# Performance work log

Measured on AMD Instinct MI355X. Metric: run time of the kernel, lower is better.

## Reference

```python
import jax, jax.numpy as jnp
import numpy as np

EPS = 1e-5


def setup_inputs() -> dict:
    key = jax.random.key(0)
    k1, k2, k3, k4 = jax.random.split(key, 4)
    B, C, H, W = 4, 64, 128, 256
    Hg, Wg = 512, 1024
    NC = 19  # num_class; loop also covers ignore label 255 -> NC+1 entries
    x = jax.random.normal(k1, (B, C, H, W), dtype=jnp.float32)
    gt = jax.random.randint(k2, (B, Hg, Wg), 0, 19).astype(jnp.int32)
    eps_mu = jax.random.normal(k3, (NC + 1, B, C), dtype=jnp.float32)
    eps_std = jax.random.normal(k4, (NC + 1, B, C), dtype=jnp.float32)
    return {"x": x, "gt": gt, "eps_mu": eps_mu, "eps_std": eps_std}


def _sqrtvar(t):
    # torch .var(dim=0) is unbiased (ddof=1); repeat over batch is just broadcast
    return jnp.sqrt(jnp.var(t, axis=0, ddof=1, keepdims=True) + EPS)


def reference(x, gt, eps_mu, eps_std):
    B, C, H, W = x.shape
    NC1 = eps_mu.shape[0]  # num_class + 1 (ignore label 255)
    Hg, Wg = gt.shape[1], gt.shape[2]
    # nearest resize of the (binary) mask == compare on nearest-resized labels
    # torch F.interpolate nearest: src = floor(dst * in/out)
    ih = (jnp.arange(H) * Hg) // H
    iw = (jnp.arange(W) * Wg) // W
    gt_r = gt[:, ih[:, None], iw[None, :]]  # [B,H,W]
    class_ids = jnp.concatenate(
        [jnp.arange(NC1 - 1), jnp.array([255])]).astype(gt.dtype)

    def per_class(carry, inp):
        cid, emu, estd = inp
        mask = (gt_r == cid).astype(x.dtype)[:, None]  # [B,1,H,W]
        mx = x * mask
        npx = jnp.sum(mask, axis=(2, 3))               # [B,1]
        npx = jnp.where(npx == 0, jnp.ones_like(npx), npx)
        mean = jnp.sum(mx, axis=(2, 3)) / npx          # [B,C] == mean*wh/npx
        var = jnp.sum((mask * (mx - mean[:, :, None, None])) ** 2,
                      axis=(2, 3)) / npx
        std = jnp.sqrt(var + EPS)                      # [B,C]
        beta = mean + emu * _sqrtvar(mean)
        gamma = std + estd * _sqrtvar(std)
        xn = (mx - mean[:, :, None, None]) / std[:, :, None, None]
        out = mask * (xn * gamma[:, :, None, None] + beta[:, :, None, None])
        return carry + out, None

    class_x, _ = jax.lax.scan(per_class, jnp.zeros_like(x),
                              (class_ids, eps_mu, eps_std))
    return class_x
```

## Files before the change

kernel.cpp:

```cpp
#include <hip/hip_runtime.h>

#define EPS 1e-5f
constexpr int B = 4, C = 64, H = 128, W = 256;
constexpr int Hg = 512, Wg = 1024;
constexpr int NC = 19;
constexpr int HW = H * W;
constexpr int HW4 = HW / 4;

__global__ __launch_bounds__(256) void k_pack(const int* __restrict__ gt,
                                              unsigned int* __restrict__ gt_p,
                                              int* __restrict__ counts_pb) {
  __shared__ int hist[NC];
  int t = threadIdx.x;
  if (t < NC) hist[t] = 0;
  __syncthreads();
  int R = blockIdx.x * 4 + (t >> 6);
  int ws = t & 63;
  int b = R >> 7, h = R & 127;
  const int* row = gt + (size_t)(b * Hg + h * 4) * Wg;
  unsigned int c0 = (unsigned int)row[ws * 16 + 0];
  unsigned int c1 = (unsigned int)row[ws * 16 + 4];
  unsigned int c2 = (unsigned int)row[ws * 16 + 8];
  unsigned int c3 = (unsigned int)row[ws * 16 + 12];
  gt_p[R * 64 + ws] = c0 | (c1 << 8) | (c2 << 16) | (c3 << 24);
  atomicAdd(&hist[c0], 1); atomicAdd(&hist[c1], 1);
  atomicAdd(&hist[c2], 1); atomicAdd(&hist[c3], 1);
  __syncthreads();
  if (t < NC) counts_pb[t * 128 + blockIdx.x] = hist[t];
}

__global__ __launch_bounds__(256, 4) void k_stats(const float* __restrict__ x,
                                                  const unsigned int* __restrict__ gt_p,
                                                  const int* __restrict__ counts_pb,
                                                  float2* __restrict__ par,
                                                  int* __restrict__ counts) {
  int t = threadIdx.x;
  int plane = blockIdx.x >> 2;
  int q = blockIdx.x & 3;
  int b = plane >> 6, c = plane & 63;

  if (c == 0 && q == 0 && t < NC) {
    const int4* cp = (const int4*)&counts_pb[t * 128 + b * 32];
    int s = 0;
#pragma unroll
    for (int j = 0; j < 8; j++) { int4 cv = cp[j]; s += cv.x + cv.y + cv.z + cv.w; }
    counts[b * NC + t] = s;
  }

  float accS[NC], accQ[NC];
#pragma unroll
  for (int k = 0; k < NC; k++) { accS[k] = 0.f; accQ[k] = 0.f; }

  const float4* xp = (const float4*)x + (size_t)plane * (HW / 4) + q * 2048;
  const unsigned int* gp = gt_p + (size_t)b * HW4 + q * 2048;
  for (int j = 0; j < 8; j++) {
    int i = j * 256 + t;
    float4 v = xp[i];
    unsigned int g = gp[i];
    int c0 = g & 255, c1 = (g >> 8) & 255, c2 = (g >> 16) & 255, c3 = g >> 24;
#pragma unroll
    for (int k = 0; k < NC; k++) {
      float m0 = (c0 == k) ? v.x : 0.f;
      float m1 = (c1 == k) ? v.y : 0.f;
      float m2 = (c2 == k) ? v.z : 0.f;
      float m3 = (c3 == k) ? v.w : 0.f;
      accS[k] += (m0 + m1) + (m2 + m3);
      accQ[k] += fmaf(m0, m0, fmaf(m1, m1, fmaf(m2, m2, m3 * m3)));
    }
  }

#pragma unroll
  for (int k = 0; k < NC; k++) {
    float s = accS[k], qq = accQ[k];
    for (int m = 32; m >= 1; m >>= 1) {
      s  += __shfl_xor(s, m, 64);
      qq += __shfl_xor(qq, m, 64);
    }
    accS[k] = s; accQ[k] = qq;
  }
  if ((t & 63) == 0) {
    int w = t >> 6;
#pragma unroll
    for (int k = 0; k < NC; k++) {
      int e = (k * B + b) * C + c;
      par[e * 16 + q * 4 + w] = make_float2(accS[k], accQ[k]);
    }
  }
}

__global__ __launch_bounds__(256) void k_apply(const float* __restrict__ x,
                                               const unsigned int* __restrict__ gt_p,
                                               const float2* __restrict__ par,
                                               const int* __restrict__ counts,
                                               const float* __restrict__ eps_mu,
                                               const float* __restrict__ eps_std,
                                               float* __restrict__ out) {
  __shared__ float2 tab[NC];
  int t = threadIdx.x;
  int plane = blockIdx.x >> 2;
  int q = blockIdx.x & 3;
  int b = plane >> 6, c = plane & 63;
  const float4* xp = (const float4*)x + (size_t)plane * (HW / 4) + q * 2048;
  const unsigned int* gp = gt_p + (size_t)b * HW4 + q * 2048;
  float4* op = (float4*)out + (size_t)plane * (HW / 4) + q * 2048;

  float4 v0 = xp[t];
  unsigned int g0 = gp[t];

  if (t < NC) {
    float mean[B], stdv[B];
    float msum = 0.f, ssum = 0.f;
#pragma unroll
    for (int bb = 0; bb < B; bb++) {
      int cnt = counts[bb * NC + t];
      float n = cnt > 0 ? (float)cnt : 1.f;
      const float4* pp = (const float4*)&par[((t * B + bb) * C + c) * 16];
      float s = 0.f, qq = 0.f;
#pragma unroll
      for (int j = 0; j < 8; j++) { float4 p = pp[j]; s += p.x + p.z; qq += p.y + p.w; }
      float m = s / n;
      float var = qq / n - m * m;
      var = var > 0.f ? var : 0.f;
      mean[bb] = m;
      stdv[bb] = sqrtf(var + EPS);
      msum += m; ssum += stdv[bb];
    }
    float mbar = msum * 0.25f, sbar = ssum * 0.25f;
    float vm = 0.f, vs = 0.f;
#pragma unroll
    for (int bb = 0; bb < B; bb++) {
      float dm = mean[bb] - mbar; vm += dm * dm;
      float ds = stdv[bb] - sbar; vs += ds * ds;
    }
    float sqvm = sqrtf(vm * (1.f / 3.f) + EPS);
    float sqvs = sqrtf(vs * (1.f / 3.f) + EPS);
    int e = (t * B + b) * C + c;
    float beta  = mean[b] + eps_mu[e]  * sqvm;
    float gamma = stdv[b] + eps_std[e] * sqvs;
    float sc = gamma / stdv[b];
    tab[t] = make_float2(sc, beta - mean[b] * sc);
  }
  __syncthreads();

  {
    float2 a0 = tab[g0 & 255], a1 = tab[(g0 >> 8) & 255];
    float2 a2 = tab[(g0 >> 16) & 255], a3 = tab[g0 >> 24];
    float4 o;
    o.x = fmaf(v0.x, a0.x, a0.y);
    o.y = fmaf(v0.y, a1.x, a1.y);
    o.z = fmaf(v0.z, a2.x, a2.y);
    o.w = fmaf(v0.w, a3.x, a3.y);
    op[t] = o;
  }
  for (int j = 1; j < 8; j++) {
    int i = j * 256 + t;
    float4 v = xp[i];
    unsigned int g = gp[i];
    float2 a0 = tab[g & 255], a1 = tab[(g >> 8) & 255];
    float2 a2 = tab[(g >> 16) & 255], a3 = tab[g >> 24];
    float4 o;
    o.x = fmaf(v.x, a0.x, a0.y);
    o.y = fmaf(v.y, a1.x, a1.y);
    o.z = fmaf(v.z, a2.x, a2.y);
    o.w = fmaf(v.w, a3.x, a3.y);
    op[i] = o;
  }
}

extern "C" void kernel_launch(void* const* d_in, const int* in_sizes, int n_in,
                              void* d_out, int out_size, void* d_ws, size_t ws_size,
                              hipStream_t stream) {
  const float* x       = (const float*)d_in[0];
  const int*   gt      = (const int*)  d_in[1];
  const float* eps_mu  = (const float*)d_in[2];
  const float* eps_std = (const float*)d_in[3];
  float* out = (float*)d_out;

  char* ws = (char*)d_ws;
  unsigned int* gt_p     = (unsigned int*)(ws);
  int*          counts_pb= (int*)   (ws + 131072);
  int*          counts   = (int*)   (ws + 140800);
  float2*       par      = (float2*)(ws + 141104);

  hipLaunchKernelGGL(k_pack,  dim3(B * H / 4), dim3(256), 0, stream, gt, gt_p, counts_pb);
  hipLaunchKernelGGL(k_stats, dim3(B * C * 4), dim3(256), 0, stream,
                     x, gt_p, counts_pb, par, counts);
  hipLaunchKernelGGL(k_apply, dim3(B * C * 4), dim3(256), 0, stream,
                     x, gt_p, par, counts, eps_mu, eps_std, out);
}
```

Before: 119.8 us.

## Fuse pack, stats and apply into one cooperative kernel with grid syncs

Merges the three kernels into a single cooperative launch of 512 blocks. Two grid-wide barriers replace the kernel boundaries, and each block now handles half a plane instead of a quarter. The goal is to cut launch gaps between kernels and to keep each block's slice of x warm in cache between the stats pass and the apply pass. In exchange it adds cooperative-launch constraints and grid.sync cost, and there are fewer blocks to hide latency.

```diff
diff --git a/kernel.cpp b/kernel.cpp
--- a/kernel.cpp
+++ b/kernel.cpp
@@ -1,4 +1,7 @@
 #include <hip/hip_runtime.h>
+#include <hip/hip_cooperative_groups.h>
+
+namespace cg = cooperative_groups;
 
 #define EPS 1e-5f
 constexpr int B = 4, C = 64, H = 128, W = 256;
@@ -7,39 +10,44 @@
 constexpr int HW = H * W;
 constexpr int HW4 = HW / 4;
 
-__global__ __launch_bounds__(256) void k_pack(const int* __restrict__ gt,
-                                              unsigned int* __restrict__ gt_p,
-                                              int* __restrict__ counts_pb) {
+__global__ __launch_bounds__(256, 2) void k_fused(const float* __restrict__ x,
+                                                  const int* __restrict__ gt,
+                                                  const float* __restrict__ eps_mu,
+                                                  const float* __restrict__ eps_std,
+                                                  float* __restrict__ out,
+                                                  unsigned int* __restrict__ gt_p,
+                                                  int* __restrict__ counts_pb,
+                                                  int* __restrict__ counts,
+                                                  float2* __restrict__ par) {
+  cg::grid_group grid = cg::this_grid();
   __shared__ int hist[NC];
+  __shared__ float2 tab[NC];
   int t = threadIdx.x;
-  if (t < NC) hist[t] = 0;
-  __syncthreads();
-  int R = blockIdx.x * 4 + (t >> 6);
-  int ws = t & 63;
-  int b = R >> 7, h = R & 127;
-  const int* row = gt + (size_t)(b * Hg + h * 4) * Wg;
-  unsigned int c0 = (unsigned int)row[ws * 16 + 0];
-  unsigned int c1 = (unsigned int)row[ws * 16 + 4];
-  unsigned int c2 = (unsigned int)row[ws * 16 + 8];
-  unsigned int c3 = (unsigned int)row[ws * 16 + 12];
-  gt_p[R * 64 + ws] = c0 | (c1 << 8) | (c2 << 16) | (c3 << 24);
-  atomicAdd(&hist[c0], 1); atomicAdd(&hist[c1], 1);
-  atomicAdd(&hist[c2], 1); atomicAdd(&hist[c3], 1);
-  __syncthreads();
-  if (t < NC) counts_pb[t * 128 + blockIdx.x] = hist[t];
-}
+  int blk = blockIdx.x;
+  int plane = blk >> 1;
+  int half = blk & 1;
+  int b = plane >> 6, c = plane & 63;
+  int lane = t & 63, w = t >> 6;
 
-__global__ __launch_bounds__(256, 4) void k_stats(const float* __restrict__ x,
-                                                  const unsigned int* __restrict__ gt_p,
-                                                  const int* __restrict__ counts_pb,
-                                                  float2* __restrict__ par,
-                                                  int* __restrict__ counts) {
-  int t = threadIdx.x;
-  int plane = blockIdx.x >> 2;
-  int q = blockIdx.x & 3;
-  int b = plane >> 6, c = plane & 63;
+  if (blk < 128) {
+    if (t < NC) hist[t] = 0;
+    __syncthreads();
+    int R = blk * 4 + w;
+    int bb = R >> 7, h = R & 127;
+    const int* row = gt + (size_t)(bb * Hg + h * 4) * Wg;
+    unsigned int c0 = (unsigned int)row[lane * 16 + 0];
+    unsigned int c1 = (unsigned int)row[lane * 16 + 4];
+    unsigned int c2 = (unsigned int)row[lane * 16 + 8];
+    unsigned int c3 = (unsigned int)row[lane * 16 + 12];
+    gt_p[R * 64 + lane] = c0 | (c1 << 8) | (c2 << 16) | (c3 << 24);
+    atomicAdd(&hist[c0], 1); atomicAdd(&hist[c1], 1);
+    atomicAdd(&hist[c2], 1); atomicAdd(&hist[c3], 1);
+    __syncthreads();
+    if (t < NC) counts_pb[t * 128 + blk] = hist[t];
+  }
+  grid.sync();
 
-  if (c == 0 && q == 0 && t < NC) {
+  if (c == 0 && half == 0 && t < NC) {
     const int4* cp = (const int4*)&counts_pb[t * 128 + b * 32];
     int s = 0;
 #pragma unroll
@@ -51,9 +59,9 @@
 #pragma unroll
   for (int k = 0; k < NC; k++) { accS[k] = 0.f; accQ[k] = 0.f; }
 
-  const float4* xp = (const float4*)x + (size_t)plane * (HW / 4) + q * 2048;
-  const unsigned int* gp = gt_p + (size_t)b * HW4 + q * 2048;
-  for (int j = 0; j < 8; j++) {
+  const float4* xp = (const float4*)x + (size_t)plane * (HW / 4) + half * 4096;
+  const unsigned int* gp = gt_p + (size_t)b * HW4 + half * 4096;
+  for (int j = 0; j < 16; j++) {
     int i = j * 256 + t;
     float4 v = xp[i];
     unsigned int g = gp[i];
@@ -68,7 +76,6 @@
       accQ[k] += fmaf(m0, m0, fmaf(m1, m1, fmaf(m2, m2, m3 * m3)));
     }
   }
-
 #pragma unroll
   for (int k = 0; k < NC; k++) {
     float s = accS[k], qq = accQ[k];
@@ -78,32 +85,16 @@
     }
     accS[k] = s; accQ[k] = qq;
   }
-  if ((t & 63) == 0) {
-    int w = t >> 6;
+  if (lane == 0) {
 #pragma unroll
     for (int k = 0; k < NC; k++) {
       int e = (k * B + b) * C + c;
-      par[e * 16 + q * 4 + w] = make_float2(accS[k], accQ[k]);
+      par[e * 8 + half * 4 + w] = make_float2(accS[k], accQ[k]);
     }
   }
-}
+  grid.sync();
 
-__global__ __launch_bounds__(256) void k_apply(const float* __restrict__ x,
-                                               const unsigned int* __restrict__ gt_p,
-                                               const float2* __restrict__ par,
-                                               const int* __restrict__ counts,
-                                               const float* __restrict__ eps_mu,
-                                               const float* __restrict__ eps_std,
-                                               float* __restrict__ out) {
-  __shared__ float2 tab[NC];
-  int t = threadIdx.x;
-  int plane = blockIdx.x >> 2;
-  int q = blockIdx.x & 3;
-  int b = plane >> 6, c = plane & 63;
-  const float4* xp = (const float4*)x + (size_t)plane * (HW / 4) + q * 2048;
-  const unsigned int* gp = gt_p + (size_t)b * HW4 + q * 2048;
-  float4* op = (float4*)out + (size_t)plane * (HW / 4) + q * 2048;
-
+  float4* op = (float4*)out + (size_t)plane * (HW / 4) + half * 4096;
   float4 v0 = xp[t];
   unsigned int g0 = gp[t];
 
@@ -114,10 +105,10 @@
     for (int bb = 0; bb < B; bb++) {
       int cnt = counts[bb * NC + t];
       float n = cnt > 0 ? (float)cnt : 1.f;
-      const float4* pp = (const float4*)&par[((t * B + bb) * C + c) * 16];
+      const float4* pp = (const float4*)&par[((t * B + bb) * C + c) * 8];
       float s = 0.f, qq = 0.f;
 #pragma unroll
-      for (int j = 0; j < 8; j++) { float4 p = pp[j]; s += p.x + p.z; qq += p.y + p.w; }
+      for (int j = 0; j < 4; j++) { float4 p = pp[j]; s += p.x + p.z; qq += p.y + p.w; }
       float m = s / n;
       float var = qq / n - m * m;
       var = var > 0.f ? var : 0.f;
@@ -152,7 +143,7 @@
     o.w = fmaf(v0.w, a3.x, a3.y);
     op[t] = o;
   }
-  for (int j = 1; j < 8; j++) {
+  for (int j = 1; j < 16; j++) {
     int i = j * 256 + t;
     float4 v = xp[i];
     unsigned int g = gp[i];
@@ -182,9 +173,9 @@
   int*          counts   = (int*)   (ws + 140800);
   float2*       par      = (float2*)(ws + 141104);
 
-  hipLaunchKernelGGL(k_pack,  dim3(B * H / 4), dim3(256), 0, stream, gt, gt_p, counts_pb);
-  hipLaunchKernelGGL(k_stats, dim3(B * C * 4), dim3(256), 0, stream,
-                     x, gt_p, counts_pb, par, counts);
-  hipLaunchKernelGGL(k_apply, dim3(B * C * 4), dim3(256), 0, stream,
-                     x, gt_p, par, counts, eps_mu, eps_std, out);
+  void* args[] = { (void*)&x, (void*)&gt, (void*)&eps_mu, (void*)&eps_std,
+                   (void*)&out, (void*)&gt_p, (void*)&counts_pb, (void*)&counts,
+                   (void*)&par };
+  hipLaunchCooperativeKernel((const void*)k_fused, dim3(512), dim3(256),
+                             args, 0, stream);
 }
```

Result: slower. 238.8 us (+99.3%).

## Accumulate per-class stats via LDS scatter histogram and nontemporal output stores

Applied to the files above, without the earlier changes.

k_stats drops the per-thread 19-class register accumulators, where every element was masked against all classes. Each thread now does a read-modify-write into a per-thread slot of a shared float2 histogram indexed by class. The per-class reduction becomes a wave-parallel sum over LDS, and the partial-result layout shrinks from 16 to 4 entries per element, which k_apply reads accordingly. k_apply also switches output writes to nontemporal stores. This removes the roughly 19x compare/select ALU work, but it costs about 38KB of LDS per block (limiting occupancy) and adds dependent LDS read-modify-write latency.

```diff
diff --git a/kernel.cpp b/kernel.cpp
--- a/kernel.cpp
+++ b/kernel.cpp
@@ -6,6 +6,8 @@
 constexpr int NC = 19;
 constexpr int HW = H * W;
 constexpr int HW4 = HW / 4;
+
+typedef float f32x4 __attribute__((ext_vector_type(4)));
 
 __global__ __launch_bounds__(256) void k_pack(const int* __restrict__ gt,
                                               unsigned int* __restrict__ gt_p,
@@ -29,12 +31,14 @@
   if (t < NC) counts_pb[t * 128 + blockIdx.x] = hist[t];
 }
 
-__global__ __launch_bounds__(256, 4) void k_stats(const float* __restrict__ x,
-                                                  const unsigned int* __restrict__ gt_p,
-                                                  const int* __restrict__ counts_pb,
-                                                  float2* __restrict__ par,
-                                                  int* __restrict__ counts) {
+__global__ __launch_bounds__(256) void k_stats(const float* __restrict__ x,
+                                               const unsigned int* __restrict__ gt_p,
+                                               const int* __restrict__ counts_pb,
+                                               float2* __restrict__ par,
+                                               int* __restrict__ counts) {
+  __shared__ float2 acc[NC * 256];
   int t = threadIdx.x;
+  for (int k = t; k < NC * 256; k += 256) acc[k] = make_float2(0.f, 0.f);
   int plane = blockIdx.x >> 2;
   int q = blockIdx.x & 3;
   int b = plane >> 6, c = plane & 63;
@@ -46,10 +50,7 @@
     for (int j = 0; j < 8; j++) { int4 cv = cp[j]; s += cv.x + cv.y + cv.z + cv.w; }
     counts[b * NC + t] = s;
   }
-
-  float accS[NC], accQ[NC];
-#pragma unroll
-  for (int k = 0; k < NC; k++) { accS[k] = 0.f; accQ[k] = 0.f; }
+  __syncthreads();
 
   const float4* xp = (const float4*)x + (size_t)plane * (HW / 4) + q * 2048;
   const unsigned int* gp = gt_p + (size_t)b * HW4 + q * 2048;
@@ -58,32 +59,29 @@
     float4 v = xp[i];
     unsigned int g = gp[i];
     int c0 = g & 255, c1 = (g >> 8) & 255, c2 = (g >> 16) & 255, c3 = g >> 24;
-#pragma unroll
-    for (int k = 0; k < NC; k++) {
-      float m0 = (c0 == k) ? v.x : 0.f;
-      float m1 = (c1 == k) ? v.y : 0.f;
-      float m2 = (c2 == k) ? v.z : 0.f;
-      float m3 = (c3 == k) ? v.w : 0.f;
-      accS[k] += (m0 + m1) + (m2 + m3);
-      accQ[k] += fmaf(m0, m0, fmaf(m1, m1, fmaf(m2, m2, m3 * m3)));
-    }
+    float2 a;
+    a = acc[c0 * 256 + t]; a.x += v.x; a.y += v.x * v.x; acc[c0 * 256 + t] = a;
+    a = acc[c1 * 256 + t]; a.x += v.y; a.y += v.y * v.y; acc[c1 * 256 + t] = a;
+    a = acc[c2 * 256 + t]; a.x += v.z; a.y += v.z * v.z; acc[c2 * 256 + t] = a;
+    a = acc[c3 * 256 + t]; a.x += v.w; a.y += v.w * v.w; acc[c3 * 256 + t] = a;
   }
+  __syncthreads();
 
-#pragma unroll
-  for (int k = 0; k < NC; k++) {
-    float s = accS[k], qq = accQ[k];
+  int w = t >> 6, lane = t & 63;
+  for (int k = w; k < NC; k += 4) {
+    float2 a0 = acc[k * 256 + lane];
+    float2 a1 = acc[k * 256 + 64 + lane];
+    float2 a2 = acc[k * 256 + 128 + lane];
+    float2 a3 = acc[k * 256 + 192 + lane];
+    float s  = a0.x + a1.x + a2.x + a3.x;
+    float qq = a0.y + a1.y + a2.y + a3.y;
     for (int m = 32; m >= 1; m >>= 1) {
       s  += __shfl_xor(s, m, 64);
       qq += __shfl_xor(qq, m, 64);
     }
-    accS[k] = s; accQ[k] = qq;
-  }
-  if ((t & 63) == 0) {
-    int w = t >> 6;
-#pragma unroll
-    for (int k = 0; k < NC; k++) {
+    if (lane == 0) {
       int e = (k * B + b) * C + c;
-      par[e * 16 + q * 4 + w] = make_float2(accS[k], accQ[k]);
+      par[e * 4 + q] = make_float2(s, qq);
     }
   }
 }
@@ -102,7 +100,7 @@
   int b = plane >> 6, c = plane & 63;
   const float4* xp = (const float4*)x + (size_t)plane * (HW / 4) + q * 2048;
   const unsigned int* gp = gt_p + (size_t)b * HW4 + q * 2048;
-  float4* op = (float4*)out + (size_t)plane * (HW / 4) + q * 2048;
+  f32x4* op = (f32x4*)((float4*)out + (size_t)plane * (HW / 4) + q * 2048);
 
   float4 v0 = xp[t];
   unsigned int g0 = gp[t];
@@ -114,10 +112,10 @@
     for (int bb = 0; bb < B; bb++) {
       int cnt = counts[bb * NC + t];
       float n = cnt > 0 ? (float)cnt : 1.f;
-      const float4* pp = (const float4*)&par[((t * B + bb) * C + c) * 16];
-      float s = 0.f, qq = 0.f;
-#pragma unroll
-      for (int j = 0; j < 8; j++) { float4 p = pp[j]; s += p.x + p.z; qq += p.y + p.w; }
+      const float4* pp = (const float4*)&par[((t * B + bb) * C + c) * 4];
+      float4 p0 = pp[0], p1 = pp[1];
+      float s  = (p0.x + p0.z) + (p1.x + p1.z);
+      float qq = (p0.y + p0.w) + (p1.y + p1.w);
       float m = s / n;
       float var = qq / n - m * m;
       var = var > 0.f ? var : 0.f;
@@ -145,12 +143,12 @@
   {
     float2 a0 = tab[g0 & 255], a1 = tab[(g0 >> 8) & 255];
     float2 a2 = tab[(g0 >> 16) & 255], a3 = tab[g0 >> 24];
-    float4 o;
+    f32x4 o;
     o.x = fmaf(v0.x, a0.x, a0.y);
     o.y = fmaf(v0.y, a1.x, a1.y);
     o.z = fmaf(v0.z, a2.x, a2.y);
     o.w = fmaf(v0.w, a3.x, a3.y);
-    op[t] = o;
+    __builtin_nontemporal_store(o, &op[t]);
   }
   for (int j = 1; j < 8; j++) {
     int i = j * 256 + t;
@@ -158,12 +156,12 @@
     unsigned int g = gp[i];
     float2 a0 = tab[g & 255], a1 = tab[(g >> 8) & 255];
     float2 a2 = tab[(g >> 16) & 255], a3 = tab[g >> 24];
-    float4 o;
+    f32x4 o;
     o.x = fmaf(v.x, a0.x, a0.y);
     o.y = fmaf(v.y, a1.x, a1.y);
     o.z = fmaf(v.z, a2.x, a2.y);
     o.w = fmaf(v.w, a3.x, a3.y);
-    op[i] = o;
+    __builtin_nontemporal_store(o, &op[i]);
   }
 }
 
```

Result: faster. 101.4 us (-15.4%).
